# Kernel optimization log

Hardware: AMD Instinct MI355X
Metric: run time of the kernel (lower is better)

The kernel has to match this reference:

```python
import jax, jax.numpy as jnp
import numpy as np

DT_MIN, DT_MAX = 0.001, 0.1
CHUNK = 64


def setup_inputs() -> dict:
    key = jax.random.key(0)
    ks = jax.random.split(key, 8)
    b, L, D = 2, 4096, 1024
    d_inner, d_state, nheads, K = 2048, 128, 32, 4
    conv_dim = d_inner + 2 * d_state            # 2304
    d_in_proj = 2 * d_inner + 2 * d_state + nheads  # 4384
    f32 = jnp.float32
    return {
        'x': jax.random.normal(ks[0], (b, L, D), f32),
        'in_proj_w': jax.random.normal(ks[1], (d_in_proj, D), f32) * (D ** -0.5),
        'conv_w': jax.random.normal(ks[2], (conv_dim, K), f32) * 0.3,
        'conv_b': jnp.zeros((conv_dim,), f32),
        'dt_bias': jax.random.normal(ks[3], (nheads,), f32) * 0.5,
        'A_log': jnp.log(jax.random.uniform(ks[4], (nheads,), f32, 1.0, 16.0)),
        'D_skip': jnp.ones((nheads,), f32),
        'norm_w': jnp.ones((d_inner,), f32),
        'out_proj_w': jax.random.normal(ks[5], (D, d_inner), f32) * (d_inner ** -0.5),
        'ln_w': jnp.ones((D,), f32),
        'ln_b': jnp.zeros((D,), f32),
    }


def reference(x, in_proj_w, conv_w, conv_b, dt_bias, A_log, D_skip, norm_w, out_proj_w, ln_w, ln_b):
    b, L, d_model = x.shape
    d_inner = norm_w.shape[0]
    nheads = A_log.shape[0]
    hd = d_inner // nheads                      # headdim = 64
    conv_dim = conv_w.shape[0]
    d_state = (conv_dim - d_inner) // 2
    Q = CHUNK
    c = L // Q

    # ---- Mamba2 in_proj ----
    zxbcdt = jnp.einsum('bld,kd->blk', x, in_proj_w)
    z = zxbcdt[..., :d_inner]                                   # gate
    xBC = zxbcdt[..., d_inner:d_inner + conv_dim]
    dt_raw = zxbcdt[..., d_inner + conv_dim:]                   # (b,L,h)

    # ---- causal depthwise conv1d (kernel 4) + SiLU ----
    K = conv_w.shape[1]
    xp = jnp.pad(xBC, ((0, 0), (K - 1, 0), (0, 0)))
    conv = sum(xp[:, k:k + L, :] * conv_w[:, k] for k in range(K)) + conv_b
    xBC = jax.nn.silu(conv)
    x_ssm = xBC[..., :d_inner]
    Bm = xBC[..., d_inner:d_inner + d_state]                    # (b,L,n)
    Cm = xBC[..., d_inner + d_state:]                           # (b,L,n)

    # ---- bounded dt (sigmoid, per SSMBlock fix) ----
    dt = DT_MIN + (DT_MAX - DT_MIN) * jax.nn.sigmoid(dt_raw + dt_bias)  # (b,L,h)
    A = -jnp.exp(A_log)                                          # (h,)

    # ---- chunked SSD selective scan ----
    xh = x_ssm.reshape(b, c, Q, nheads, hd)
    dtc = dt.reshape(b, c, Q, nheads)
    x_dt = xh * dtc[..., None]
    dA = jnp.einsum('bcqh,h->bhcq', dtc, A)
    Acum = jnp.cumsum(dA, axis=-1)                               # (b,h,c,Q)
    Bc = Bm.reshape(b, c, Q, d_state)
    Cc = Cm.reshape(b, c, Q, d_state)

    # intra-chunk (diagonal blocks)
    seg = Acum[..., :, None] - Acum[..., None, :]                # (b,h,c,Q,Q)
    mask = jnp.tril(jnp.ones((Q, Q), bool))
    Lmat = jnp.exp(jnp.where(mask, seg, -jnp.inf))
    Yd = jnp.einsum('bcqn,bcsn,bhcqs,bcshp->bcqhp', Cc, Bc, Lmat, x_dt)

    # chunk end-states
    decay_states = jnp.exp(Acum[..., -1:] - Acum)                # (b,h,c,Q)
    states = jnp.einsum('bcqn,bhcq,bcqhp->bchpn', Bc, decay_states, x_dt)
    chunk_decay = jnp.exp(Acum[..., -1])                         # (b,h,c)

    def step(carry, inp):
        st, dec = inp
        return dec[..., None, None] * carry + st, carry

    _, prevs = jax.lax.scan(
        step, jnp.zeros((b, nheads, hd, d_state), x.dtype),
        (jnp.moveaxis(states, 1, 0), jnp.moveaxis(chunk_decay, 2, 0)))
    prevs = jnp.moveaxis(prevs, 0, 1)                            # (b,c,h,p,n)

    # inter-chunk contribution
    Yo = jnp.einsum('bcqn,bchpn,bhcq->bcqhp', Cc, prevs, jnp.exp(Acum))

    Y = (Yd + Yo).reshape(b, L, nheads, hd) + D_skip[None, None, :, None] * xh.reshape(b, L, nheads, hd)
    y = Y.reshape(b, L, d_inner)

    # ---- gated RMSNorm + out_proj ----
    y = y * jax.nn.silu(z)
    y = y * jax.lax.rsqrt(jnp.mean(y * y, axis=-1, keepdims=True) + 1e-5) * norm_w
    out = jnp.einsum('bli,di->bld', y, out_proj_w)

    # ---- SSMBlock: LayerNorm + (eval-mode dropout) + residual ----
    mu = jnp.mean(out, axis=-1, keepdims=True)
    var = jnp.mean((out - mu) ** 2, axis=-1, keepdims=True)
    ln = (out - mu) * jax.lax.rsqrt(var + 1e-5) * ln_w + ln_b
    return x + ln
```

## Files before the change

### kernel.cpp

```cpp
#include <hip/hip_runtime.h>
#include <math.h>

#define BSZ     2
#define LEN     4096
#define DMODEL  1024
#define DINNER  2048
#define DSTATE  128
#define NHEADS  32
#define HDIM    64
#define CONVDIM 2304
#define QC      64
#define NCHUNK  64
#define ROWS    (BSZ*LEN)
#define SDIM    (HDIM*DSTATE)
#define PB      136
#define PT      72
#define CGRP    (CONVDIM/8)

typedef __attribute__((ext_vector_type(8))) short short8;
typedef __attribute__((ext_vector_type(4))) float f32x4;

__device__ __forceinline__ float silu_(float x){ return x / (1.0f + expf(-x)); }
__device__ __forceinline__ float sigm_(float x){ return 1.0f / (1.0f + expf(-x)); }
__device__ __forceinline__ float bf2f(unsigned short u){
    return __uint_as_float(((unsigned int)u) << 16);
}
__device__ __forceinline__ unsigned short f2bf(float f){
    unsigned int u = __float_as_uint(f);
    u = (u + 0x7fffu + ((u >> 16) & 1u)) >> 16;
    return (unsigned short)u;
}

__device__ __forceinline__ int swzcol(int row, int col) {
    return ((((col >> 3) ^ (row >> 3)) & 7) << 3) | (col & 7);
}
__device__ __forceinline__ int swzblk(int row, int blk) {
    return (((blk ^ (row >> 3)) & 7) << 3);
}

__device__ __forceinline__ void gload16(const void* g, void* l) {
    __builtin_amdgcn_global_load_lds(
        (const __attribute__((address_space(1))) unsigned int*)g,
        (__attribute__((address_space(3))) unsigned int*)l, 16, 0, 0);
}

__global__ __launch_bounds__(256) void cast_bf16(const float* __restrict__ src,
                                                 unsigned short* __restrict__ dst,
                                                 int n4) {
    const int i = blockIdx.x * 256 + threadIdx.x;
    if (i >= n4) return;
    const float4 v = *(const float4*)(src + (size_t)i * 4);
    ushort4 o;
    o.x = f2bf(v.x); o.y = f2bf(v.y); o.z = f2bf(v.z); o.w = f2bf(v.w);
    *(ushort4*)(dst + (size_t)i * 4) = o;
}

__device__ __forceinline__ void stage_half(const unsigned short* __restrict__ G,
                                           void* ldsbase, int w, int lane,
                                           size_t rowbase, int lda, int kcol) {
#pragma unroll
    for (int u = 0; u < 2; u++) {
        const int f = w * 128 + u * 64 + lane;
        const int r = f >> 3;
        const int cl = (lane & 7) ^ (lane >> 3);
        gload16(G + rowbase + (size_t)r * lda + kcol + cl * 8,
                (char*)ldsbase + f * 16);
    }
}

#define WAITV(n) asm volatile("s_waitcnt vmcnt(" #n ")" ::: "memory")
#define LGKM0    asm volatile("s_waitcnt lgkmcnt(0)" ::: "memory")
#define BARRIER  do { asm volatile("" ::: "memory"); \
                      __builtin_amdgcn_s_barrier();  \
                      asm volatile("" ::: "memory"); } while (0)

#define READ_A(dst, buf, half)                                                \
    _Pragma("unroll")                                                         \
    for (int fr = 0; fr < 4; fr++) {                                          \
        const int r_ = (w & 1) * 64 + fr * 16 + l16;                          \
        _Pragma("unroll")                                                     \
        for (int s = 0; s < 2; s++)                                           \
            dst[fr][s] = *(const short8*)((const char*)&lds[buf][0][half][0]  \
                + r_ * 128 + (((s * 4 + quad) ^ rx7) << 4));                  \
    }
#define READ_B(dst, buf, half)                                                \
    _Pragma("unroll")                                                         \
    for (int fc = 0; fc < 2; fc++) {                                          \
        const int r_ = (w >> 1) * 32 + fc * 16 + l16;                         \
        _Pragma("unroll")                                                     \
        for (int s = 0; s < 2; s++)                                           \
            dst[fc][s] = *(const short8*)((const char*)&lds[buf][1][half][0]  \
                + r_ * 128 + (((s * 4 + quad) ^ rx7) << 4));                  \
    }
#define MFMA16(g, af, bfv)                                                    \
    __builtin_amdgcn_s_setprio(1);                                            \
    _Pragma("unroll")                                                         \
    for (int s = 0; s < 2; s++)                                               \
        _Pragma("unroll")                                                     \
        for (int fr = 0; fr < 4; fr++)                                        \
            _Pragma("unroll")                                                 \
            for (int fc = 0; fc < 2; fc++)                                    \
                acc[g][fr][fc] = __builtin_amdgcn_mfma_f32_16x16x32_bf16(     \
                    af[fr][s], bfv[fc][s], acc[g][fr][fc], 0, 0, 0);          \
    __builtin_amdgcn_s_setprio(0);

template<bool BF16OUT>
__global__ __launch_bounds__(512, 2) void gemm8p(const unsigned short* __restrict__ A,
                                                 const unsigned short* __restrict__ B,
                                                 void* __restrict__ C0,
                                                 void* __restrict__ C1,
                                                 int N, int Kfull, int Ks,
                                                 int gx, int nwg1) {
    __shared__ unsigned short lds[2][2][2][8192];
    const int tid = threadIdx.x;
    const int w = tid >> 6, lane = tid & 63;
    const int quad = lane >> 4, l16 = lane & 15;
    const int rx7 = l16 & 7;

    const int nwg = gridDim.x;
    const int id = blockIdx.x;
    const int q8 = nwg >> 3, r8 = nwg & 7;
    const int xcd = id & 7, idx = id >> 3;
    const int wg = (xcd < r8 ? xcd * (q8 + 1) : r8 * (q8 + 1) + (xcd - r8) * q8) + idx;
    const int sid = wg / nwg1;
    const int wgl = wg % nwg1;
    const int m0 = (wgl / gx) * 256, n0 = (wgl % gx) * 256;
    const int kbase = sid * Ks;
    void* Cout = sid ? C1 : C0;

    const size_t a0r = (size_t)m0 * Kfull;
    const size_t a1r = (size_t)(m0 + 128) * Kfull;
    const size_t b0r = (size_t)n0 * Kfull;
    const size_t b1r = (size_t)(n0 + 128) * Kfull;

    f32x4 acc[4][4][2];
#pragma unroll
    for (int g = 0; g < 4; g++)
#pragma unroll
        for (int i = 0; i < 4; i++)
#pragma unroll
            for (int j = 0; j < 2; j++) acc[g][i][j] = (f32x4){0.f, 0.f, 0.f, 0.f};

    const int NT = Ks >> 6;
    stage_half(A, &lds[0][0][0][0], w, lane, a0r, Kfull, kbase);
    stage_half(B, &lds[0][1][0][0], w, lane, b0r, Kfull, kbase);
    stage_half(A, &lds[0][0][1][0], w, lane, a1r, Kfull, kbase);
    stage_half(B, &lds[0][1][1][0], w, lane, b1r, Kfull, kbase);
    stage_half(A, &lds[1][0][0][0], w, lane, a0r, Kfull, kbase + 64);
    stage_half(B, &lds[1][1][0][0], w, lane, b0r, Kfull, kbase + 64);
    stage_half(A, &lds[1][0][1][0], w, lane, a1r, Kfull, kbase + 64);
    WAITV(6); BARRIER;

    short8 af0[4][2], af1[4][2], bf0[2][2], bf1[2][2];
    for (int p = 0; p < (NT >> 1) - 1; p++) {
        const int kb1 = kbase + (2 * p + 1) * 64;
        const int ka2 = kbase + (2 * p + 2) * 64;
        const int kb2 = kbase + (2 * p + 3) * 64;
        READ_A(af0, 0, 0); READ_B(bf0, 0, 0);
        stage_half(B, &lds[1][1][1][0], w, lane, b1r, Kfull, kb1);
        BARRIER; MFMA16(0, af0, bf0); LGKM0; BARRIER;
        READ_A(af1, 0, 1);
        stage_half(A, &lds[0][0][0][0], w, lane, a0r, Kfull, ka2);
        BARRIER; MFMA16(1, af1, bf0); LGKM0; BARRIER;
        READ_B(bf1, 0, 1);
        stage_half(B, &lds[0][1][0][0], w, lane, b0r, Kfull, ka2);
        BARRIER; MFMA16(2, af0, bf1); LGKM0; BARRIER;
        stage_half(A, &lds[0][0][1][0], w, lane, a1r, Kfull, ka2);
        WAITV(6); BARRIER; MFMA16(3, af1, bf1); LGKM0; BARRIER;
        READ_A(af0, 1, 0); READ_B(bf0, 1, 0);
        stage_half(B, &lds[0][1][1][0], w, lane, b1r, Kfull, ka2);
        BARRIER; MFMA16(0, af0, bf0); LGKM0; BARRIER;
        READ_A(af1, 1, 1);
        stage_half(A, &lds[1][0][0][0], w, lane, a0r, Kfull, kb2);
        BARRIER; MFMA16(1, af1, bf0); LGKM0; BARRIER;
        READ_B(bf1, 1, 1);
        stage_half(B, &lds[1][1][0][0], w, lane, b0r, Kfull, kb2);
        BARRIER; MFMA16(2, af0, bf1); LGKM0; BARRIER;
        stage_half(A, &lds[1][0][1][0], w, lane, a1r, Kfull, kb2);
        WAITV(6); BARRIER; MFMA16(3, af1, bf1); LGKM0; BARRIER;
    }
    READ_A(af0, 0, 0); READ_B(bf0, 0, 0);
    stage_half(B, &lds[1][1][1][0], w, lane, b1r, Kfull, kbase + (NT - 1) * 64);
    MFMA16(0, af0, bf0);
    READ_A(af1, 0, 1);
    MFMA16(1, af1, bf0);
    READ_B(bf1, 0, 1);
    MFMA16(2, af0, bf1);
    MFMA16(3, af1, bf1);
    WAITV(0); LGKM0; BARRIER;
    READ_A(af0, 1, 0); READ_B(bf0, 1, 0);
    MFMA16(0, af0, bf0);
    READ_A(af1, 1, 1);
    MFMA16(1, af1, bf0);
    READ_B(bf1, 1, 1);
    MFMA16(2, af0, bf1);
    MFMA16(3, af1, bf1);

#pragma unroll
    for (int g = 0; g < 4; g++) {
        const int qm = g & 1, qn = g >> 1;
        const int mb = m0 + qm * 128 + (w & 1) * 64;
        const int nb2 = n0 + qn * 128 + (w >> 1) * 32;
#pragma unroll
        for (int fr = 0; fr < 4; fr++)
#pragma unroll
            for (int fc = 0; fc < 2; fc++) {
                const int n = nb2 + fc * 16 + l16;
#pragma unroll
                for (int rr = 0; rr < 4; rr++) {
                    const int m = mb + fr * 16 + quad * 4 + rr;
                    if (BF16OUT)
                        ((unsigned short*)Cout)[(size_t)m * N + n] = f2bf(acc[g][fr][fc][rr]);
                    else
                        ((float*)Cout)[(size_t)m * N + n] = acc[g][fr][fc][rr];
                }
            }
    }
}

__global__ __launch_bounds__(256) void dtproj_mfma(const unsigned short* __restrict__ A,
                                                   const unsigned short* __restrict__ W,
                                                   const float* __restrict__ bias,
                                                   float* __restrict__ dtb,
                                                   int K) {
    __shared__ unsigned short As[128 * 32];
    __shared__ unsigned short Bs[32 * 32];
    const int tid = threadIdx.x;
    const int wave = tid >> 6, lane = tid & 63;
    const int quad = lane >> 4, l16 = lane & 15;
    const int m0 = blockIdx.x * 128;

    f32x4 acc[2][2];
#pragma unroll
    for (int i = 0; i < 2; i++)
#pragma unroll
        for (int j = 0; j < 2; j++) acc[i][j] = (f32x4){0.f, 0.f, 0.f, 0.f};

    for (int kt = 0; kt < K; kt += 32) {
#pragma unroll
        for (int u = 0; u < 2; u++) {
            const int f = u * 256 + tid;
            const int row = f >> 2, ke = (f & 3) * 8;
            gload16(A + (size_t)(m0 + row) * K + kt + ke, ((char*)As) + f * 16);
        }
        if (tid < 128) {
            const int row = tid >> 2, ke = (tid & 3) * 8;
            gload16(W + (size_t)row * K + kt + ke, ((char*)Bs) + tid * 16);
        }
        __syncthreads();
        short8 af[2], bfr[2];
#pragma unroll
        for (int i = 0; i < 2; i++)
            af[i] = *(const short8*)((const char*)As + (wave * 32 + i * 16 + l16) * 64 + quad * 16);
#pragma unroll
        for (int j = 0; j < 2; j++)
            bfr[j] = *(const short8*)((const char*)Bs + (j * 16 + l16) * 64 + quad * 16);
#pragma unroll
        for (int i = 0; i < 2; i++)
#pragma unroll
            for (int j = 0; j < 2; j++)
                acc[i][j] = __builtin_amdgcn_mfma_f32_16x16x32_bf16(
                    af[i], bfr[j], acc[i][j], 0, 0, 0);
        __syncthreads();
    }
#pragma unroll
    for (int i = 0; i < 2; i++)
#pragma unroll
        for (int j = 0; j < 2; j++) {
            const int h = j * 16 + l16;
            const float bh = bias[h];
#pragma unroll
            for (int r = 0; r < 4; r++) {
                const int m = m0 + wave * 32 + i * 16 + quad * 4 + r;
                dtb[(size_t)m * NHEADS + h] =
                    0.001f + 0.099f * sigm_(acc[i][j][r] + bh);
            }
        }
}

__global__ __launch_bounds__(256) void conv_silu_w(const unsigned short* __restrict__ xbc,
                                                   const float* __restrict__ cw,
                                                   const float* __restrict__ cb,
                                                   unsigned short* __restrict__ xssm,
                                                   unsigned short* __restrict__ Bb,
                                                   unsigned short* __restrict__ Cb) {
    const int idx = blockIdx.x * 256 + threadIdx.x;
    const int g = idx % CGRP;
    const int rowblk = idx / CGRP;
    const long row0 = (long)rowblk * 4;
    const int lbase = (int)(row0 & (LEN - 1));
    const int j0 = g * 8;

    float4 wv[8];
    float cbv[8];
#pragma unroll
    for (int e = 0; e < 8; e++) {
        wv[e] = *(const float4*)(cw + (size_t)(j0 + e) * 4);
        cbv[e] = cb[j0 + e];
    }

    short8 win[4];
    const short8 zero8 = (short8){0, 0, 0, 0, 0, 0, 0, 0};
#pragma unroll
    for (int t = 0; t < 3; t++) {
        const int lr = lbase - 3 + t;
        win[t] = (lr >= 0) ? *(const short8*)(xbc + (row0 - 3 + t) * CONVDIM + j0)
                           : zero8;
    }
#pragma unroll
    for (int i = 0; i < 4; i++) {
        win[3] = *(const short8*)(xbc + (row0 + i) * CONVDIM + j0);
        short8 o;
#pragma unroll
        for (int e = 0; e < 8; e++) {
            float acc = cbv[e];
            acc += bf2f((unsigned short)win[0][e]) * wv[e].x;
            acc += bf2f((unsigned short)win[1][e]) * wv[e].y;
            acc += bf2f((unsigned short)win[2][e]) * wv[e].z;
            acc += bf2f((unsigned short)win[3][e]) * wv[e].w;
            o[e] = (short)f2bf(silu_(acc));
        }
        const long row = row0 + i;
        if (j0 < DINNER)
            *(short8*)(xssm + row * DINNER + j0) = o;
        else if (j0 < DINNER + DSTATE)
            *(short8*)(Bb + row * DSTATE + (j0 - DINNER)) = o;
        else
            *(short8*)(Cb + row * DSTATE + (j0 - DINNER - DSTATE)) = o;
        win[0] = win[1]; win[1] = win[2]; win[2] = win[3];
    }
}

__global__ __launch_bounds__(64) void acum_kernel(const float* __restrict__ dtb,
                                                  const float* __restrict__ A_log,
                                                  float* __restrict__ Acum) {
    const int c = blockIdx.x, h = blockIdx.y, b = blockIdx.z;
    const int q = threadIdx.x;
    const float Av = -expf(A_log[h]);
    float v = dtb[((size_t)b * LEN + c * QC + q) * NHEADS + h] * Av;
#pragma unroll
    for (int off = 1; off < 64; off <<= 1) {
        const float n = __shfl_up(v, off, 64);
        if (q >= off) v += n;
    }
    Acum[(((size_t)b * NHEADS + h) * NCHUNK + c) * QC + q] = v;
}

__global__ __launch_bounds__(256) void chunk_mfma(const unsigned short* __restrict__ xssm,
                                                  const unsigned short* __restrict__ Bb,
                                                  const unsigned short* __restrict__ Cb,
                                                  const float* __restrict__ dtb,
                                                  const float* __restrict__ Acum,
                                                  const float* __restrict__ Dskip,
                                                  unsigned short* __restrict__ Y,
                                                  unsigned short* __restrict__ states) {
    const int c = blockIdx.x, h = blockIdx.y, b = blockIdx.z;
    const int tid = threadIdx.x;
    const int wave = tid >> 6, lane = tid & 63;
    const int quad = lane >> 4, l16 = lane & 15;

    __shared__ __attribute__((aligned(16))) unsigned short Bsh[8704];
    __shared__ __attribute__((aligned(16))) unsigned short Csh[9216];
    __shared__ __attribute__((aligned(16))) unsigned short xTs[4608];
    __shared__ float ac[QC], dts[QC], decs[QC];

    const size_t rowbase = (size_t)b * LEN + c * QC;
    if (tid < QC) {
        ac[tid]  = Acum[(((size_t)b * NHEADS + h) * NCHUNK + c) * QC + tid];
        dts[tid] = dtb[(rowbase + tid) * NHEADS + h];
    }
#pragma unroll
    for (int u = 0; u < 4; u++) {
        const int vi = u * 256 + tid;
        const int s = vi >> 4, n0 = (vi & 15) * 8;
        *(short8*)&Bsh[s * PB + n0] = *(const short8*)(Bb + (rowbase + s) * DSTATE + n0);
        *(short8*)&Csh[s * PB + n0] = *(const short8*)(Cb + (rowbase + s) * DSTATE + n0);
    }
#pragma unroll
    for (int u = 0; u < 2; u++) {
        const int vi = u * 256 + tid;
        const int q = vi >> 3, p0 = (vi & 7) * 8;
        const short8 v = *(const short8*)(xssm + (rowbase + q) * DINNER + h * HDIM + p0);
#pragma unroll
        for (int j = 0; j < 8; j++) {
            const int p = p0 + j;
            xTs[p * PT + swzcol(p, q)] = (unsigned short)v[j];
        }
    }
    __syncthreads();
    if (tid < QC) decs[tid] = expf(ac[QC - 1] - ac[tid]) * dts[tid];

    f32x4 S[4];
#pragma unroll
    for (int j = 0; j < 4; j++) S[j] = (f32x4){0.f, 0.f, 0.f, 0.f};
    const int qa = wave * 16 + l16;
#pragma unroll
    for (int ks = 0; ks < 4; ks++) {
        const short8 a = *(const short8*)&Csh[qa * PB + ks * 32 + quad * 8];
#pragma unroll
        for (int j = 0; j < 4; j++) {
            const short8 bb = *(const short8*)&Bsh[(j * 16 + l16) * PB + ks * 32 + quad * 8];
            S[j] = __builtin_amdgcn_mfma_f32_16x16x32_bf16(a, bb, S[j], 0, 0, 0);
        }
    }
    unsigned short slv[4][4];
#pragma unroll
    for (int j = 0; j < 4; j++)
#pragma unroll
        for (int r = 0; r < 4; r++) {
            const int q = wave * 16 + quad * 4 + r, s = j * 16 + l16;
            const float v = (s <= q) ? S[j][r] * expf(ac[q] - ac[s]) * dts[s] : 0.f;
            slv[j][r] = f2bf(v);
        }
    __syncthreads();

    {
        const int sin = lane & 7;
        const int ng  = lane >> 3;
#pragma unroll
        for (int so = 0; so < 2; so++) {
            const int s = (wave * 2 + so) * 8 + sin;
            const float d = decs[s];
            const int cbk = s >> 3;
#pragma unroll
            for (int nh = 0; nh < 2; nh++) {
                const int noct = ng + 8 * nh;
                const int colphys = (((cbk ^ noct) & 7) << 3) | (s & 7);
#pragma unroll
                for (int j = 0; j < 8; j++) {
                    const int n = noct * 8 + ((j + sin) & 7);
                    Csh[n * PT + colphys] = f2bf(bf2f(Bsh[s * PB + n]) * d);
                }
            }
        }
    }
    __syncthreads();

#pragma unroll
    for (int j = 0; j < 4; j++)
#pragma unroll
        for (int r = 0; r < 4; r++) {
            const int row = wave * 16 + quad * 4 + r;
            const int col = j * 16 + l16;
            Bsh[row * PT + swzcol(row, col)] = slv[j][r];
        }
    __syncthreads();

    f32x4 yd[4];
#pragma unroll
    for (int j = 0; j < 4; j++) yd[j] = (f32x4){0.f, 0.f, 0.f, 0.f};
#pragma unroll
    for (int ks = 0; ks < 2; ks++) {
        const int blk = ks * 4 + quad;
        const short8 a = *(const short8*)&Bsh[qa * PT + swzblk(qa, blk)];
#pragma unroll
        for (int j = 0; j < 4; j++) {
            const int row = j * 16 + l16;
            const short8 xb = *(const short8*)&xTs[row * PT + swzblk(row, blk)];
            yd[j] = __builtin_amdgcn_mfma_f32_16x16x32_bf16(a, xb, yd[j], 0, 0, 0);
        }
    }
    const float Dh = Dskip[h];
#pragma unroll
    for (int j = 0; j < 4; j++)
#pragma unroll
        for (int r = 0; r < 4; r++) {
            const int q = wave * 16 + quad * 4 + r, p = j * 16 + l16;
            const float v = yd[j][r] + Dh * bf2f(xTs[p * PT + swzcol(p, q)]);
            Y[(rowbase + q) * DINNER + h * HDIM + p] = f2bf(v);
        }

    f32x4 st[8];
#pragma unroll
    for (int j = 0; j < 8; j++) st[j] = (f32x4){0.f, 0.f, 0.f, 0.f};
#pragma unroll
    for (int ks = 0; ks < 2; ks++) {
        const int blk = ks * 4 + quad;
        const short8 a = *(const short8*)&xTs[qa * PT + swzblk(qa, blk)];
#pragma unroll
        for (int j = 0; j < 8; j++) {
            const int row = j * 16 + l16;
            const short8 bb = *(const short8*)&Csh[row * PT + swzblk(row, blk)];
            st[j] = __builtin_amdgcn_mfma_f32_16x16x32_bf16(a, bb, st[j], 0, 0, 0);
        }
    }
    const size_t sbase = (((size_t)b * NHEADS + h) * NCHUNK + c) * SDIM;
#pragma unroll
    for (int j = 0; j < 8; j++)
#pragma unroll
        for (int r = 0; r < 4; r++) {
            const int p = wave * 16 + quad * 4 + r, n = j * 16 + l16;
            states[sbase + (size_t)p * DSTATE + n] = f2bf(st[j][r]);
        }
}

__global__ __launch_bounds__(256) void scan_kernel(unsigned short* __restrict__ states,
                                                   const float* __restrict__ Acum) {
    __shared__ float dec[NCHUNK];
    const int bh = blockIdx.y;
    const int pn = blockIdx.x * 256 + threadIdx.x;
    if (threadIdx.x < NCHUNK)
        dec[threadIdx.x] = expf(Acum[((size_t)bh * NCHUNK + threadIdx.x) * QC + (QC - 1)]);
    __syncthreads();
    float carry = 0.f;
    const size_t base = (size_t)bh * NCHUNK * SDIM + pn;
    for (int c = 0; c < NCHUNK; c++) {
        const size_t idx = base + (size_t)c * SDIM;
        const float s = bf2f(states[idx]);
        states[idx] = f2bf(carry);
        carry = dec[c] * carry + s;
    }
}

__global__ __launch_bounds__(256) void yo_mfma(const unsigned short* __restrict__ Cb,
                                               const unsigned short* __restrict__ prevs,
                                               const float* __restrict__ Acum,
                                               unsigned short* __restrict__ Y) {
    const int c = blockIdx.x, h = blockIdx.y, b = blockIdx.z;
    const int tid = threadIdx.x;
    const int wave = tid >> 6, lane = tid & 63;
    const int quad = lane >> 4, l16 = lane & 15;
    __shared__ __attribute__((aligned(16))) unsigned short Csh[8704];
    __shared__ __attribute__((aligned(16))) unsigned short Psh[8704];
    __shared__ float eq[QC];
    const size_t rowbase = (size_t)b * LEN + c * QC;
    const size_t pbase = (((size_t)b * NHEADS + h) * NCHUNK + c) * SDIM;
    if (tid < QC)
        eq[tid] = expf(Acum[(((size_t)b * NHEADS + h) * NCHUNK + c) * QC + tid]);
#pragma unroll
    for (int u = 0; u < 4; u++) {
        const int vi = u * 256 + tid;
        const int r = vi >> 4, n0 = (vi & 15) * 8;
        *(short8*)&Csh[r * PB + n0] = *(const short8*)(Cb + (rowbase + r) * DSTATE + n0);
        *(short8*)&Psh[r * PB + n0] = *(const short8*)(prevs + pbase + (size_t)r * DSTATE + n0);
    }
    __syncthreads();

    f32x4 acc[4];
#pragma unroll
    for (int j = 0; j < 4; j++) acc[j] = (f32x4){0.f, 0.f, 0.f, 0.f};
    const int qa = wave * 16 + l16;
#pragma unroll
    for (int ks = 0; ks < 4; ks++) {
        const short8 a = *(const short8*)&Csh[qa * PB + ks * 32 + quad * 8];
#pragma unroll
        for (int j = 0; j < 4; j++) {
            const short8 bb = *(const short8*)&Psh[(j * 16 + l16) * PB + ks * 32 + quad * 8];
            acc[j] = __builtin_amdgcn_mfma_f32_16x16x32_bf16(a, bb, acc[j], 0, 0, 0);
        }
    }
#pragma unroll
    for (int j = 0; j < 4; j++)
#pragma unroll
        for (int r = 0; r < 4; r++) {
            const int q = wave * 16 + quad * 4 + r, p = j * 16 + l16;
            const size_t off = (rowbase + q) * DINNER + h * HDIM + p;
            Y[off] = f2bf(bf2f(Y[off]) + eq[q] * acc[j][r]);
        }
}

__global__ __launch_bounds__(256) void gate_rms(const unsigned short* __restrict__ Y,
                                                const unsigned short* __restrict__ zbf,
                                                const float* __restrict__ nw,
                                                unsigned short* __restrict__ ybf) {
    const int r = blockIdx.x, tid = threadIdx.x;
    float4 yv[2];
    float ss = 0.f;
#pragma unroll
    for (int u = 0; u < 2; u++) {
        const int col = u * 1024 + tid * 4;
        const ushort4 y4 = *(const ushort4*)(Y + (size_t)r * DINNER + col);
        const ushort4 z4 = *(const ushort4*)(zbf + (size_t)r * DINNER + col);
        float4 y;
        y.x = bf2f(y4.x) * silu_(bf2f(z4.x)); y.y = bf2f(y4.y) * silu_(bf2f(z4.y));
        y.z = bf2f(y4.z) * silu_(bf2f(z4.z)); y.w = bf2f(y4.w) * silu_(bf2f(z4.w));
        yv[u] = y;
        ss += y.x * y.x + y.y * y.y + y.z * y.z + y.w * y.w;
    }
#pragma unroll
    for (int off = 32; off; off >>= 1) ss += __shfl_xor(ss, off, 64);
    __shared__ float red[4];
    if ((tid & 63) == 0) red[tid >> 6] = ss;
    __syncthreads();
    ss = red[0] + red[1] + red[2] + red[3];
    const float scale = rsqrtf(ss / (float)DINNER + 1e-5f);
#pragma unroll
    for (int u = 0; u < 2; u++) {
        const int col = u * 1024 + tid * 4;
        const float4 w4 = *(const float4*)(nw + col);
        ushort4 o;
        o.x = f2bf(yv[u].x * scale * w4.x); o.y = f2bf(yv[u].y * scale * w4.y);
        o.z = f2bf(yv[u].z * scale * w4.z); o.w = f2bf(yv[u].w * scale * w4.w);
        *(ushort4*)(ybf + (size_t)r * DINNER + col) = o;
    }
}

__global__ __launch_bounds__(256) void ln_res(const float* __restrict__ outb,
                                              const float* __restrict__ part,
                                              const float* __restrict__ x,
                                              const float* __restrict__ lw,
                                              const float* __restrict__ lb,
                                              float* __restrict__ out) {
    const int r = blockIdx.x, tid = threadIdx.x;
    const int col = tid * 4;
    float4 v = *(const float4*)(outb + (size_t)r * DMODEL + col);
    const float4 pv = *(const float4*)(part + (size_t)r * DMODEL + col);
    v.x += pv.x; v.y += pv.y; v.z += pv.z; v.w += pv.w;
    float s = v.x + v.y + v.z + v.w;
    float s2 = v.x * v.x + v.y * v.y + v.z * v.z + v.w * v.w;
#pragma unroll
    for (int off = 32; off; off >>= 1) {
        s += __shfl_xor(s, off, 64);
        s2 += __shfl_xor(s2, off, 64);
    }
    __shared__ float rs[4], rs2[4];
    if ((tid & 63) == 0) { rs[tid >> 6] = s; rs2[tid >> 6] = s2; }
    __syncthreads();
    s = rs[0] + rs[1] + rs[2] + rs[3];
    s2 = rs2[0] + rs2[1] + rs2[2] + rs2[3];
    const float mu = s / (float)DMODEL;
    const float var = s2 / (float)DMODEL - mu * mu;
    const float inv = rsqrtf(var + 1e-5f);
    const float4 xw = *(const float4*)(x + (size_t)r * DMODEL + col);
    const float4 w4 = *(const float4*)(lw + col);
    const float4 b4 = *(const float4*)(lb + col);
    float4 o;
    o.x = xw.x + (v.x - mu) * inv * w4.x + b4.x;
    o.y = xw.y + (v.y - mu) * inv * w4.y + b4.y;
    o.z = xw.z + (v.z - mu) * inv * w4.z + b4.z;
    o.w = xw.w + (v.w - mu) * inv * w4.w + b4.w;
    *(float4*)(out + (size_t)r * DMODEL + col) = o;
}

extern "C" void kernel_launch(void* const* d_in, const int* in_sizes, int n_in,
                              void* d_out, int out_size, void* d_ws, size_t ws_size,
                              hipStream_t stream) {
    const float* x          = (const float*)d_in[0];
    const float* in_proj_w  = (const float*)d_in[1];
    const float* conv_w     = (const float*)d_in[2];
    const float* conv_b     = (const float*)d_in[3];
    const float* dt_bias    = (const float*)d_in[4];
    const float* A_log      = (const float*)d_in[5];
    const float* D_skip     = (const float*)d_in[6];
    const float* norm_w     = (const float*)d_in[7];
    const float* out_proj_w = (const float*)d_in[8];
    const float* ln_w       = (const float*)d_in[9];
    const float* ln_b       = (const float*)d_in[10];
    float* out = (float*)d_out;
    float* ws = (float*)d_ws;

    size_t off = 0;
    unsigned short* zbf     = (unsigned short*)(ws + off); off += (size_t)ROWS * DINNER / 2;
    unsigned short* xssm_bf = (unsigned short*)(ws + off); off += (size_t)ROWS * DINNER / 2;
    unsigned short* uni     = (unsigned short*)(ws + off); off += (size_t)ROWS * CONVDIM / 2;
    unsigned short* Bb_bf   = (unsigned short*)(ws + off); off += (size_t)ROWS * DSTATE / 2;
    unsigned short* Cb_bf   = (unsigned short*)(ws + off); off += (size_t)ROWS * DSTATE / 2;
    float* dtb   = ws + off; off += (size_t)ROWS * NHEADS;
    float* Acum  = ws + off; off += (size_t)BSZ * NHEADS * NCHUNK * QC;
    unsigned short* x_bf  = (unsigned short*)(ws + off); off += (size_t)ROWS * DMODEL / 2;
    unsigned short* wi_bf = (unsigned short*)(ws + off); off += (size_t)4384 * DMODEL / 2;
    unsigned short* wo_bf = (unsigned short*)(ws + off); off += (size_t)DMODEL * DINNER / 2;
    unsigned short* states = (unsigned short*)(ws + off); off += (size_t)BSZ * NHEADS * NCHUNK * SDIM / 2;
    float* part = ws + off; off += (size_t)ROWS * DMODEL;
    const size_t need_bytes = off * sizeof(float);
    if (ws_size < need_bytes) return;

    unsigned short* xbc_bf = uni;
    unsigned short* Ybf    = uni;
    unsigned short* ybf    = xssm_bf;

    cast_bf16<<<(ROWS * DMODEL / 4 + 255) / 256, 256, 0, stream>>>(x, x_bf, ROWS * DMODEL / 4);
    cast_bf16<<<(4384 * DMODEL / 4 + 255) / 256, 256, 0, stream>>>(in_proj_w, wi_bf, 4384 * DMODEL / 4);
    cast_bf16<<<(DMODEL * DINNER / 4 + 255) / 256, 256, 0, stream>>>(out_proj_w, wo_bf, DMODEL * DINNER / 4);

    gemm8p<true><<<(ROWS / 256) * (DINNER / 256), 512, 0, stream>>>(
        x_bf, wi_bf, zbf, nullptr, DINNER, DMODEL, DMODEL,
        DINNER / 256, (ROWS / 256) * (DINNER / 256));
    gemm8p<true><<<(ROWS / 256) * (CONVDIM / 256), 512, 0, stream>>>(
        x_bf, wi_bf + (size_t)DINNER * DMODEL, xbc_bf, nullptr, CONVDIM, DMODEL, DMODEL,
        CONVDIM / 256, (ROWS / 256) * (CONVDIM / 256));
    dtproj_mfma<<<ROWS / 128, 256, 0, stream>>>(
        x_bf, wi_bf + (size_t)(DINNER + CONVDIM) * DMODEL, dt_bias, dtb, DMODEL);

    conv_silu_w<<<(ROWS / 4) * CGRP / 256, 256, 0, stream>>>(
        xbc_bf, conv_w, conv_b, xssm_bf, Bb_bf, Cb_bf);
    acum_kernel<<<dim3(NCHUNK, NHEADS, BSZ), 64, 0, stream>>>(dtb, A_log, Acum);
    chunk_mfma<<<dim3(NCHUNK, NHEADS, BSZ), 256, 0, stream>>>(
        xssm_bf, Bb_bf, Cb_bf, dtb, Acum, D_skip, Ybf, states);
    scan_kernel<<<dim3(SDIM / 256, BSZ * NHEADS), 256, 0, stream>>>(states, Acum);
    yo_mfma<<<dim3(NCHUNK, NHEADS, BSZ), 256, 0, stream>>>(Cb_bf, states, Acum, Ybf);
    gate_rms<<<ROWS, 256, 0, stream>>>(Ybf, zbf, norm_w, ybf);

    gemm8p<false><<<2 * (ROWS / 256) * (DMODEL / 256), 512, 0, stream>>>(
        ybf, wo_bf, out, part, DMODEL, DINNER, DINNER / 2,
        DMODEL / 256, (ROWS / 256) * (DMODEL / 256));
    ln_res<<<ROWS, 256, 0, stream>>>(out, part, x, ln_w, ln_b, out);
}
```

Measured before the change: 423.3 us.

## Fuse inter-chunk state scan with Yo MFMA and split-K the dt projection

```diff
diff --git a/kernel.cpp b/kernel.cpp
--- a/kernel.cpp
+++ b/kernel.cpp
@@ -223,12 +223,14 @@
                                                    const float* __restrict__ bias,
                                                    float* __restrict__ dtb,
                                                    int K) {
-    __shared__ unsigned short As[128 * 32];
-    __shared__ unsigned short Bs[32 * 32];
+    __shared__ unsigned short As[4][2][32 * 32];
+    __shared__ unsigned short Ws[4][2][32 * 32];
+    __shared__ float red[4][32][32];
     const int tid = threadIdx.x;
-    const int wave = tid >> 6, lane = tid & 63;
+    const int w = tid >> 6, lane = tid & 63;
     const int quad = lane >> 4, l16 = lane & 15;
-    const int m0 = blockIdx.x * 128;
+    const int m0 = blockIdx.x * 32;
+    const int kbeg = w * (1024 / 4);
 
     f32x4 acc[2][2];
 #pragma unroll
@@ -236,46 +238,52 @@
 #pragma unroll
         for (int j = 0; j < 2; j++) acc[i][j] = (f32x4){0.f, 0.f, 0.f, 0.f};
 
-    for (int kt = 0; kt < K; kt += 32) {
-#pragma unroll
-        for (int u = 0; u < 2; u++) {
-            const int f = u * 256 + tid;
-            const int row = f >> 2, ke = (f & 3) * 8;
-            gload16(A + (size_t)(m0 + row) * K + kt + ke, ((char*)As) + f * 16);
-        }
-        if (tid < 128) {
-            const int row = tid >> 2, ke = (tid & 3) * 8;
-            gload16(W + (size_t)row * K + kt + ke, ((char*)Bs) + tid * 16);
-        }
-        __syncthreads();
+#define DTSTAGE(buf, kt)                                                      \
+    _Pragma("unroll")                                                         \
+    for (int u = 0; u < 2; u++) {                                             \
+        const int f = u * 64 + lane;                                          \
+        const int row = f >> 2, ke = (f & 3) * 8;                             \
+        gload16(A + (size_t)(m0 + row) * K + (kt) + ke,                       \
+                (char*)&As[w][buf][0] + f * 16);                              \
+        gload16(W + (size_t)row * K + (kt) + ke,                              \
+                (char*)&Ws[w][buf][0] + f * 16);                              \
+    }
+
+    DTSTAGE(0, kbeg);
+    int buf = 0;
+    for (int it = 0; it < 8; it++) {
+        if (it < 7) { DTSTAGE(buf ^ 1, kbeg + (it + 1) * 32); WAITV(4); }
+        else        { WAITV(0); }
         short8 af[2], bfr[2];
 #pragma unroll
         for (int i = 0; i < 2; i++)
-            af[i] = *(const short8*)((const char*)As + (wave * 32 + i * 16 + l16) * 64 + quad * 16);
+            af[i] = *(const short8*)((const char*)&As[w][buf][0] + (i * 16 + l16) * 64 + quad * 16);
 #pragma unroll
         for (int j = 0; j < 2; j++)
-            bfr[j] = *(const short8*)((const char*)Bs + (j * 16 + l16) * 64 + quad * 16);
+            bfr[j] = *(const short8*)((const char*)&Ws[w][buf][0] + (j * 16 + l16) * 64 + quad * 16);
 #pragma unroll
         for (int i = 0; i < 2; i++)
 #pragma unroll
             for (int j = 0; j < 2; j++)
                 acc[i][j] = __builtin_amdgcn_mfma_f32_16x16x32_bf16(
                     af[i], bfr[j], acc[i][j], 0, 0, 0);
-        __syncthreads();
+        buf ^= 1;
     }
 #pragma unroll
     for (int i = 0; i < 2; i++)
 #pragma unroll
-        for (int j = 0; j < 2; j++) {
-            const int h = j * 16 + l16;
-            const float bh = bias[h];
-#pragma unroll
-            for (int r = 0; r < 4; r++) {
-                const int m = m0 + wave * 32 + i * 16 + quad * 4 + r;
-                dtb[(size_t)m * NHEADS + h] =
-                    0.001f + 0.099f * sigm_(acc[i][j][r] + bh);
-            }
-        }
+        for (int j = 0; j < 2; j++)
+#pragma unroll
+            for (int r = 0; r < 4; r++)
+                red[w][i * 16 + quad * 4 + r][j * 16 + l16] = acc[i][j][r];
+    __syncthreads();
+#pragma unroll
+    for (int e = 0; e < 4; e++) {
+        const int o = tid + e * 256;
+        const int m = o >> 5, hh = o & 31;
+        const float v = red[0][m][hh] + red[1][m][hh] + red[2][m][hh] + red[3][m][hh];
+        dtb[(size_t)m0 * NHEADS + o] = 0.001f + 0.099f * sigm_(v + bias[hh]);
+    }
 }
 
 __global__ __launch_bounds__(256) void conv_silu_w(const unsigned short* __restrict__ xbc,
@@ -494,69 +502,79 @@
         }
 }
 
-__global__ __launch_bounds__(256) void scan_kernel(unsigned short* __restrict__ states,
-                                                   const float* __restrict__ Acum) {
-    __shared__ float dec[NCHUNK];
-    const int bh = blockIdx.y;
-    const int pn = blockIdx.x * 256 + threadIdx.x;
-    if (threadIdx.x < NCHUNK)
-        dec[threadIdx.x] = expf(Acum[((size_t)bh * NCHUNK + threadIdx.x) * QC + (QC - 1)]);
-    __syncthreads();
-    float carry = 0.f;
-    const size_t base = (size_t)bh * NCHUNK * SDIM + pn;
-    for (int c = 0; c < NCHUNK; c++) {
-        const size_t idx = base + (size_t)c * SDIM;
-        const float s = bf2f(states[idx]);
-        states[idx] = f2bf(carry);
-        carry = dec[c] * carry + s;
-    }
-}
-
-__global__ __launch_bounds__(256) void yo_mfma(const unsigned short* __restrict__ Cb,
-                                               const unsigned short* __restrict__ prevs,
-                                               const float* __restrict__ Acum,
-                                               unsigned short* __restrict__ Y) {
-    const int c = blockIdx.x, h = blockIdx.y, b = blockIdx.z;
+__global__ __launch_bounds__(256) void scanyo_mfma(const unsigned short* __restrict__ Cb,
+                                                   const unsigned short* __restrict__ states,
+                                                   const float* __restrict__ Acum,
+                                                   unsigned short* __restrict__ Y) {
+    const int pb = blockIdx.x;
+    const int h = blockIdx.y, b = blockIdx.z;
     const int tid = threadIdx.x;
-    const int wave = tid >> 6, lane = tid & 63;
+    const int w = tid >> 6, lane = tid & 63;
     const int quad = lane >> 4, l16 = lane & 15;
-    __shared__ __attribute__((aligned(16))) unsigned short Csh[8704];
-    __shared__ __attribute__((aligned(16))) unsigned short Psh[8704];
-    __shared__ float eq[QC];
-    const size_t rowbase = (size_t)b * LEN + c * QC;
-    const size_t pbase = (((size_t)b * NHEADS + h) * NCHUNK + c) * SDIM;
-    if (tid < QC)
-        eq[tid] = expf(Acum[(((size_t)b * NHEADS + h) * NCHUNK + c) * QC + tid]);
-#pragma unroll
-    for (int u = 0; u < 4; u++) {
-        const int vi = u * 256 + tid;
-        const int r = vi >> 4, n0 = (vi & 15) * 8;
-        *(short8*)&Csh[r * PB + n0] = *(const short8*)(Cb + (rowbase + r) * DSTATE + n0);
-        *(short8*)&Psh[r * PB + n0] = *(const short8*)(prevs + pbase + (size_t)r * DSTATE + n0);
-    }
-    __syncthreads();
-
-    f32x4 acc[4];
-#pragma unroll
-    for (int j = 0; j < 4; j++) acc[j] = (f32x4){0.f, 0.f, 0.f, 0.f};
-    const int qa = wave * 16 + l16;
-#pragma unroll
-    for (int ks = 0; ks < 4; ks++) {
-        const short8 a = *(const short8*)&Csh[qa * PB + ks * 32 + quad * 8];
-#pragma unroll
-        for (int j = 0; j < 4; j++) {
-            const short8 bb = *(const short8*)&Psh[(j * 16 + l16) * PB + ks * 32 + quad * 8];
-            acc[j] = __builtin_amdgcn_mfma_f32_16x16x32_bf16(a, bb, acc[j], 0, 0, 0);
-        }
-    }
-#pragma unroll
-    for (int j = 0; j < 4; j++)
-#pragma unroll
-        for (int r = 0; r < 4; r++) {
-            const int q = wave * 16 + quad * 4 + r, p = j * 16 + l16;
-            const size_t off = (rowbase + q) * DINNER + h * HDIM + p;
-            Y[off] = f2bf(bf2f(Y[off]) + eq[q] * acc[j][r]);
-        }
+    const size_t bh = (size_t)b * NHEADS + h;
+    const float* Ac = Acum + bh * NCHUNK * QC;
+    const size_t rowb0 = (size_t)b * LEN;
+
+    float carry[4][8];
+#pragma unroll
+    for (int s = 0; s < 4; s++)
+#pragma unroll
+        for (int j = 0; j < 8; j++) carry[s][j] = 0.f;
+
+    const unsigned short* stp = states + bh * NCHUNK * SDIM
+                              + (size_t)(pb * 16 + l16) * DSTATE + quad * 8;
+    const unsigned short* cp = Cb + (rowb0 + (size_t)w * 16 + l16) * DSTATE + quad * 8;
+
+    short8 cR[4][4], sR[4][4];
+#define LOADCH(ri, c)                                                          \
+    _Pragma("unroll")                                                          \
+    for (int s = 0; s < 4; s++) {                                              \
+        cR[ri][s] = *(const short8*)(cp + (size_t)(c) * (QC * DSTATE) + s * 32); \
+        sR[ri][s] = *(const short8*)(stp + (size_t)(c) * SDIM + s * 32);       \
+    }
+#define PROC(ri, c)                                                            \
+    {                                                                          \
+        const float dec_c = expf(Ac[(c) * QC + (QC - 1)]);                     \
+        float eqv[4];                                                          \
+        _Pragma("unroll")                                                      \
+        for (int r = 0; r < 4; r++)                                            \
+            eqv[r] = expf(Ac[(c) * QC + w * 16 + quad * 4 + r]);               \
+        short8 pv[4];                                                          \
+        _Pragma("unroll")                                                      \
+        for (int s = 0; s < 4; s++)                                            \
+            _Pragma("unroll")                                                  \
+            for (int j = 0; j < 8; j++)                                        \
+                pv[s][j] = (short)f2bf(carry[s][j]);                           \
+        f32x4 acc = (f32x4){0.f, 0.f, 0.f, 0.f};                               \
+        _Pragma("unroll")                                                      \
+        for (int s = 0; s < 4; s++)                                            \
+            acc = __builtin_amdgcn_mfma_f32_16x16x32_bf16(cR[ri][s], pv[s], acc, 0, 0, 0); \
+        _Pragma("unroll")                                                      \
+        for (int s = 0; s < 4; s++)                                            \
+            _Pragma("unroll")                                                  \
+            for (int j = 0; j < 8; j++)                                        \
+                carry[s][j] = dec_c * carry[s][j] + bf2f((unsigned short)sR[ri][s][j]); \
+        _Pragma("unroll")                                                      \
+        for (int r = 0; r < 4; r++) {                                          \
+            const size_t off = (rowb0 + (size_t)(c) * QC + w * 16 + quad * 4 + r) * DINNER \
+                             + h * HDIM + pb * 16 + l16;                       \
+            Y[off] = f2bf(bf2f(Y[off]) + eqv[r] * acc[r]);                     \
+        }                                                                      \
+    }
+
+    LOADCH(0, 0); LOADCH(1, 1); LOADCH(2, 2); LOADCH(3, 3);
+    for (int c = 0; c < NCHUNK; c += 4) {
+        PROC(0, c);
+        if (c + 4 < NCHUNK) LOADCH(0, c + 4);
+        PROC(1, c + 1);
+        if (c + 5 < NCHUNK) LOADCH(1, c + 5);
+        PROC(2, c + 2);
+        if (c + 6 < NCHUNK) LOADCH(2, c + 6);
+        PROC(3, c + 3);
+        if (c + 7 < NCHUNK) LOADCH(3, c + 7);
+    }
+#undef LOADCH
+#undef PROC
 }
 
 __global__ __launch_bounds__(256) void gate_rms(const unsigned short* __restrict__ Y,
@@ -679,7 +697,7 @@
     gemm8p<true><<<(ROWS / 256) * (CONVDIM / 256), 512, 0, stream>>>(
         x_bf, wi_bf + (size_t)DINNER * DMODEL, xbc_bf, nullptr, CONVDIM, DMODEL, DMODEL,
         CONVDIM / 256, (ROWS / 256) * (CONVDIM / 256));
-    dtproj_mfma<<<ROWS / 128, 256, 0, stream>>>(
+    dtproj_mfma<<<ROWS / 32, 256, 0, stream>>>(
         x_bf, wi_bf + (size_t)(DINNER + CONVDIM) * DMODEL, dt_bias, dtb, DMODEL);
 
     conv_silu_w<<<(ROWS / 4) * CGRP / 256, 256, 0, stream>>>(
@@ -687,8 +705,8 @@
     acum_kernel<<<dim3(NCHUNK, NHEADS, BSZ), 64, 0, stream>>>(dtb, A_log, Acum);
     chunk_mfma<<<dim3(NCHUNK, NHEADS, BSZ), 256, 0, stream>>>(
         xssm_bf, Bb_bf, Cb_bf, dtb, Acum, D_skip, Ybf, states);
-    scan_kernel<<<dim3(SDIM / 256, BSZ * NHEADS), 256, 0, stream>>>(states, Acum);
-    yo_mfma<<<dim3(NCHUNK, NHEADS, BSZ), 256, 0, stream>>>(Cb_bf, states, Acum, Ybf);
+    scanyo_mfma<<<dim3(4, NHEADS, BSZ), 256, 0, stream>>>(
+        Cb_bf, states, Acum, Ybf);
     gate_rms<<<ROWS, 256, 0, stream>>>(Ybf, zbf, norm_w, ybf);
 
     gemm8p<false><<<2 * (ROWS / 256) * (DMODEL / 256), 512, 0, stream>>>(
```

Measured after the change: 501.7 us. 18.5% more time.

## Split-K dt projection across waves and merge three cast launches

Applied to the files above, without the earlier changes.

```diff
diff --git a/kernel.cpp b/kernel.cpp
--- a/kernel.cpp
+++ b/kernel.cpp
@@ -44,15 +44,23 @@
         (__attribute__((address_space(3))) unsigned int*)l, 16, 0, 0);
 }
 
-__global__ __launch_bounds__(256) void cast_bf16(const float* __restrict__ src,
-                                                 unsigned short* __restrict__ dst,
-                                                 int n4) {
-    const int i = blockIdx.x * 256 + threadIdx.x;
-    if (i >= n4) return;
+__device__ __forceinline__ void cast4(const float* __restrict__ src,
+                                      unsigned short* __restrict__ dst, int i) {
     const float4 v = *(const float4*)(src + (size_t)i * 4);
     ushort4 o;
     o.x = f2bf(v.x); o.y = f2bf(v.y); o.z = f2bf(v.z); o.w = f2bf(v.w);
     *(ushort4*)(dst + (size_t)i * 4) = o;
+}
+
+__global__ __launch_bounds__(256) void cast3(const float* __restrict__ s0, unsigned short* __restrict__ d0, int n0,
+                                             const float* __restrict__ s1, unsigned short* __restrict__ d1, int n1,
+                                             const float* __restrict__ s2, unsigned short* __restrict__ d2, int n2) {
+    int i = blockIdx.x * 256 + threadIdx.x;
+    if (i < n0) { cast4(s0, d0, i); return; }
+    i -= n0;
+    if (i < n1) { cast4(s1, d1, i); return; }
+    i -= n1;
+    if (i < n2) cast4(s2, d2, i);
 }
 
 __device__ __forceinline__ void stage_half(const unsigned short* __restrict__ G,
@@ -223,12 +231,14 @@
                                                    const float* __restrict__ bias,
                                                    float* __restrict__ dtb,
                                                    int K) {
-    __shared__ unsigned short As[128 * 32];
-    __shared__ unsigned short Bs[32 * 32];
+    __shared__ unsigned short As[4][2][32 * 32];
+    __shared__ unsigned short Ws[4][2][32 * 32];
+    __shared__ float red[4][32][32];
     const int tid = threadIdx.x;
-    const int wave = tid >> 6, lane = tid & 63;
+    const int w = tid >> 6, lane = tid & 63;
     const int quad = lane >> 4, l16 = lane & 15;
-    const int m0 = blockIdx.x * 128;
+    const int m0 = blockIdx.x * 32;
+    const int kbeg = w * (1024 / 4);
 
     f32x4 acc[2][2];
 #pragma unroll
@@ -236,46 +246,52 @@
 #pragma unroll
         for (int j = 0; j < 2; j++) acc[i][j] = (f32x4){0.f, 0.f, 0.f, 0.f};
 
-    for (int kt = 0; kt < K; kt += 32) {
-#pragma unroll
-        for (int u = 0; u < 2; u++) {
-            const int f = u * 256 + tid;
-            const int row = f >> 2, ke = (f & 3) * 8;
-            gload16(A + (size_t)(m0 + row) * K + kt + ke, ((char*)As) + f * 16);
-        }
-        if (tid < 128) {
-            const int row = tid >> 2, ke = (tid & 3) * 8;
-            gload16(W + (size_t)row * K + kt + ke, ((char*)Bs) + tid * 16);
-        }
-        __syncthreads();
+#define DTSTAGE(buf, kt)                                                      \
+    _Pragma("unroll")                                                         \
+    for (int u = 0; u < 2; u++) {                                             \
+        const int f = u * 64 + lane;                                          \
+        const int row = f >> 2, ke = (f & 3) * 8;                             \
+        gload16(A + (size_t)(m0 + row) * K + (kt) + ke,                       \
+                (char*)&As[w][buf][0] + f * 16);                              \
+        gload16(W + (size_t)row * K + (kt) + ke,                              \
+                (char*)&Ws[w][buf][0] + f * 16);                              \
+    }
+
+    DTSTAGE(0, kbeg);
+    int buf = 0;
+    for (int it = 0; it < 8; it++) {
+        if (it < 7) { DTSTAGE(buf ^ 1, kbeg + (it + 1) * 32); WAITV(4); }
+        else        { WAITV(0); }
         short8 af[2], bfr[2];
 #pragma unroll
         for (int i = 0; i < 2; i++)
-            af[i] = *(const short8*)((const char*)As + (wave * 32 + i * 16 + l16) * 64 + quad * 16);
+            af[i] = *(const short8*)((const char*)&As[w][buf][0] + (i * 16 + l16) * 64 + quad * 16);
 #pragma unroll
         for (int j = 0; j < 2; j++)
-            bfr[j] = *(const short8*)((const char*)Bs + (j * 16 + l16) * 64 + quad * 16);
+            bfr[j] = *(const short8*)((const char*)&Ws[w][buf][0] + (j * 16 + l16) * 64 + quad * 16);
 #pragma unroll
         for (int i = 0; i < 2; i++)
 #pragma unroll
             for (int j = 0; j < 2; j++)
                 acc[i][j] = __builtin_amdgcn_mfma_f32_16x16x32_bf16(
                     af[i], bfr[j], acc[i][j], 0, 0, 0);
-        __syncthreads();
+        buf ^= 1;
     }
 #pragma unroll
     for (int i = 0; i < 2; i++)
 #pragma unroll
-        for (int j = 0; j < 2; j++) {
-            const int h = j * 16 + l16;
-            const float bh = bias[h];
-#pragma unroll
-            for (int r = 0; r < 4; r++) {
-                const int m = m0 + wave * 32 + i * 16 + quad * 4 + r;
-                dtb[(size_t)m * NHEADS + h] =
-                    0.001f + 0.099f * sigm_(acc[i][j][r] + bh);
-            }
-        }
+        for (int j = 0; j < 2; j++)
+#pragma unroll
+            for (int r = 0; r < 4; r++)
+                red[w][i * 16 + quad * 4 + r][j * 16 + l16] = acc[i][j][r];
+    __syncthreads();
+#pragma unroll
+    for (int e = 0; e < 4; e++) {
+        const int o = tid + e * 256;
+        const int m = o >> 5, hh = o & 31;
+        const float v = red[0][m][hh] + red[1][m][hh] + red[2][m][hh] + red[3][m][hh];
+        dtb[(size_t)m0 * NHEADS + o] = 0.001f + 0.099f * sigm_(v + bias[hh]);
+    }
 }
 
 __global__ __launch_bounds__(256) void conv_silu_w(const unsigned short* __restrict__ xbc,
@@ -669,9 +685,11 @@
     unsigned short* Ybf    = uni;
     unsigned short* ybf    = xssm_bf;
 
-    cast_bf16<<<(ROWS * DMODEL / 4 + 255) / 256, 256, 0, stream>>>(x, x_bf, ROWS * DMODEL / 4);
-    cast_bf16<<<(4384 * DMODEL / 4 + 255) / 256, 256, 0, stream>>>(in_proj_w, wi_bf, 4384 * DMODEL / 4);
-    cast_bf16<<<(DMODEL * DINNER / 4 + 255) / 256, 256, 0, stream>>>(out_proj_w, wo_bf, DMODEL * DINNER / 4);
+    {
+        const int n0 = ROWS * DMODEL / 4, n1 = 4384 * DMODEL / 4, n2 = DMODEL * DINNER / 4;
+        cast3<<<(n0 + n1 + n2 + 255) / 256, 256, 0, stream>>>(
+            x, x_bf, n0, in_proj_w, wi_bf, n1, out_proj_w, wo_bf, n2);
+    }
 
     gemm8p<true><<<(ROWS / 256) * (DINNER / 256), 512, 0, stream>>>(
         x_bf, wi_bf, zbf, nullptr, DINNER, DMODEL, DMODEL,
@@ -679,7 +697,7 @@
     gemm8p<true><<<(ROWS / 256) * (CONVDIM / 256), 512, 0, stream>>>(
         x_bf, wi_bf + (size_t)DINNER * DMODEL, xbc_bf, nullptr, CONVDIM, DMODEL, DMODEL,
         CONVDIM / 256, (ROWS / 256) * (CONVDIM / 256));
-    dtproj_mfma<<<ROWS / 128, 256, 0, stream>>>(
+    dtproj_mfma<<<ROWS / 32, 256, 0, stream>>>(
         x_bf, wi_bf + (size_t)(DINNER + CONVDIM) * DMODEL, dt_bias, dtb, DMODEL);
 
     conv_silu_w<<<(ROWS / 4) * CGRP / 256, 256, 0, stream>>>(
```

New measurement: 402.7 us. -4.9%, faster.
